# Kernel optimization log

Measured on AMD Instinct MI355X. Metric: run time of the kernel, lower is better.

## Reference

```python
import jax, jax.numpy as jnp
import numpy as np

DIM = 384
HEADS = 12
WIN = (2, 7, 7)
MLP_RATIO = 4.0
EPS = 1e-5


def _rel_index(Wt, Wh, Ww):
    t, h, w = np.meshgrid(np.arange(Wt), np.arange(Wh), np.arange(Ww), indexing='ij')
    coords = np.stack([t, h, w]).reshape(3, -1).T  # (N,3)
    rel = coords[:, None] - coords[None]  # (N,N,3)
    rel[..., 0] += Wt - 1
    rel[..., 1] += Wh - 1
    rel[..., 2] += Ww - 1
    rel[..., 0] *= (2 * Wh - 1) * (2 * Ww - 1)
    rel[..., 1] *= (2 * Ww - 1)
    return rel.sum(-1)  # (N,N) int


def setup_inputs() -> dict:
    key = jax.random.key(0)
    ks = jax.random.split(key, 16)
    d = DIM
    hdim = int(d * MLP_RATIO)
    Wt, Wh, Ww = WIN
    table_size = (2 * Wt - 1) * (2 * Wh - 1) * (2 * Ww - 1)
    s = lambda fan: 1.0 / np.sqrt(fan)
    return {
        'x': jax.random.normal(ks[0], (2, 8, 56, 56, d), jnp.float32),
        'norm1_g': jnp.ones((d,), jnp.float32),
        'norm1_b': jnp.zeros((d,), jnp.float32),
        'qkv_w': jax.random.normal(ks[1], (d, 3 * d), jnp.float32) * s(d),
        'qkv_b': jnp.zeros((3 * d,), jnp.float32),
        'proj_w': jax.random.normal(ks[2], (d, d), jnp.float32) * s(d),
        'proj_b': jnp.zeros((d,), jnp.float32),
        'bias_table': jax.random.normal(ks[3], (table_size, HEADS), jnp.float32) * 0.02,
        'norm2_g': jnp.ones((d,), jnp.float32),
        'norm2_b': jnp.zeros((d,), jnp.float32),
        'fc1_w': jax.random.normal(ks[4], (d, hdim), jnp.float32) * s(d),
        'fc1_b': jnp.zeros((hdim,), jnp.float32),
        'fc2_w': jax.random.normal(ks[5], (hdim, d), jnp.float32) * s(hdim),
        'fc2_b': jnp.zeros((d,), jnp.float32),
        'rel_index': jnp.asarray(_rel_index(*WIN), jnp.int32),
    }


def _ln(x, g, b):
    mu = x.mean(-1, keepdims=True)
    var = ((x - mu) ** 2).mean(-1, keepdims=True)
    return (x - mu) * jax.lax.rsqrt(var + EPS) * g + b


def _window_partition(x, win):
    B, T, H, W, C = x.shape
    Wt, Wh, Ww = win
    x = x.reshape(B, T // Wt, Wt, H // Wh, Wh, W // Ww, Ww, C)
    x = x.transpose(0, 1, 3, 5, 2, 4, 6, 7)
    return x.reshape(-1, Wt * Wh * Ww, C)


def _window_reverse(win_x, win, B, T, H, W):
    Wt, Wh, Ww = win
    C = win_x.shape[-1]
    x = win_x.reshape(B, T // Wt, H // Wh, W // Ww, Wt, Wh, Ww, C)
    x = x.transpose(0, 1, 4, 2, 5, 3, 6, 7)
    return x.reshape(B, T, H, W, C)


def reference(x, norm1_g, norm1_b, qkv_w, qkv_b, proj_w, proj_b, bias_table,
              norm2_g, norm2_b, fc1_w, fc1_b, fc2_w, fc2_b, rel_index):
    B, T, H, W, C = x.shape
    Wt, Wh, Ww = WIN
    N = Wt * Wh * Ww
    shift = (Wt // 2, Wh // 2, Ww // 2)
    head_dim = C // HEADS
    scale = head_dim ** -0.5

    shortcut = x
    h = _ln(x, norm1_g, norm1_b)
    h = jnp.roll(h, shift=(-shift[0], -shift[1], -shift[2]), axis=(1, 2, 3))
    # dims chosen divisible by window -> no padding branch
    wins = _window_partition(h, WIN)  # (BnW, N, C)
    BnW = wins.shape[0]

    qkv = wins @ qkv_w + qkv_b  # (BnW, N, 3C)
    qkv = qkv.reshape(BnW, N, 3, HEADS, head_dim).transpose(2, 0, 3, 1, 4)
    q, k, v = qkv[0] * scale, qkv[1], qkv[2]  # (BnW, H, N, d)

    bias = bias_table[rel_index.reshape(-1)].reshape(N, N, HEADS).transpose(2, 0, 1)
    attn = jnp.einsum('bhnd,bhmd->bhnm', q, k) + bias[None]
    attn = jax.nn.softmax(attn, axis=-1)
    out = jnp.einsum('bhnm,bhmd->bhnd', attn, v)
    out = out.transpose(0, 2, 1, 3).reshape(BnW, N, C)
    out = out @ proj_w + proj_b

    h = _window_reverse(out.reshape(-1, Wt, Wh, Ww, C), WIN, B, T, H, W)
    h = jnp.roll(h, shift=shift, axis=(1, 2, 3))
    x = shortcut + h

    h2 = _ln(x, norm2_g, norm2_b)
    h2 = jax.nn.gelu(h2 @ fc1_w + fc1_b, approximate=False) @ fc2_w + fc2_b
    return x + h2
```

## Files before the change

kernel.cpp:

```cpp
#include <hip/hip_runtime.h>
#include <cstdint>
#include <cstddef>


typedef __bf16 bf16x8 __attribute__((ext_vector_type(8)));
typedef __bf16 bf16x4 __attribute__((ext_vector_type(4)));
typedef float f32x4 __attribute__((ext_vector_type(4)));

#define DIM 384
#define QKV_DIM 1152
#define HID 1536
#define NHEADS 12
#define NTOK 50176
#define NWIN 512

__device__ __forceinline__ void gload16(const void* g, void* s) {
  __builtin_amdgcn_global_load_lds(
      (const __attribute__((address_space(1))) void*)g,
      (__attribute__((address_space(3))) void*)s, 16, 0, 0);
}

__global__ __launch_bounds__(256) void build_tokmap_k(int* __restrict__ map) {
  int t = blockIdx.x * 256 + threadIdx.x;
  if (t >= NTOK) return;
  int win = t / 98, n = t - win * 98;
  int b = win >> 8, tw = (win >> 6) & 3, hw = (win >> 3) & 7, ww = win & 7;
  int dt = n / 49; int rem = n - dt * 49; int dh = rem / 7, dw = rem - dh * 7;
  int t0 = (tw * 2 + dt + 1) & 7;
  int h0 = hw * 7 + dh + 3; if (h0 >= 56) h0 -= 56;
  int w0 = ww * 7 + dw + 3; if (w0 >= 56) w0 -= 56;
  map[t] = ((b * 8 + t0) * 56 + h0) * 56 + w0;
}

__global__ __launch_bounds__(256) void expand_biasp_k(const float* __restrict__ table,
                                                      const int* __restrict__ rel,
                                                      float* __restrict__ out) {
  int e = blockIdx.x * 256 + threadIdx.x;
  if (e >= NHEADS * 49 * 256) return;
  int r = e & 3, l = (e >> 2) & 63;
  int rest = e >> 8;
  int ni = rest % 7, mi = (rest / 7) % 7, h = rest / 49;
  int i = mi * 16 + (l >> 4) * 4 + r;
  int j = ni * 16 + (l & 15);
  float v;
  if (j >= 98) v = -1e30f;
  else if (i >= 98) v = 0.f;
  else v = table[rel[i * 98 + j] * NHEADS + h];
  out[e] = v;
}

__global__ __launch_bounds__(256) void transpose_w_k(const float* __restrict__ W,
                                                     __bf16* __restrict__ WT,
                                                     int K, int N, int scaleCols, float scale) {
  int e = blockIdx.x * 256 + threadIdx.x;
  if (e >= K * N) return;
  int n = e / K, k = e - n * K;
  float v = W[(size_t)k * N + n];
  if (n < scaleCols) v *= scale;
  WT[e] = (__bf16)v;
}

__global__ __launch_bounds__(256) void scale_bias_k(const float* __restrict__ b,
                                                    float* __restrict__ out,
                                                    int n, int scaleCols, float scale) {
  int e = blockIdx.x * 256 + threadIdx.x;
  if (e >= n) return;
  out[e] = b[e] * (e < scaleCols ? scale : 1.0f);
}

__global__ __launch_bounds__(384) void vtrans_k(const __bf16* __restrict__ qkv,
                                                __bf16* __restrict__ vt) {
  int win = blockIdx.x, t = threadIdx.x;
  const __bf16* base = qkv + (size_t)win * 98 * QKV_DIM + 768 + t;
  __bf16* orow = vt + ((size_t)win * 384 + t) * 128;
  #pragma unroll
  for (int c = 0; c < 16; ++c) {
    bf16x8 pk;
    #pragma unroll
    for (int e2 = 0; e2 < 8; ++e2) {
      int tok = c * 8 + e2;
      pk[e2] = (tok < 98) ? base[(size_t)tok * QKV_DIM] : (__bf16)0.f;
    }
    *(bf16x8*)(orow + c * 8) = pk;
  }
}

__global__ __launch_bounds__(256) void ln_k(const float* __restrict__ x,
                                            const float* __restrict__ g,
                                            const float* __restrict__ bta,
                                            __bf16* __restrict__ out,
                                            const int* __restrict__ map) {
  int w = threadIdx.x >> 6, l = threadIdx.x & 63;
  int tok = blockIdx.x * 4 + w;
  int src = map ? map[tok] : tok;
  const float* row = x + (size_t)src * DIM;
  float v[6]; float s = 0.f;
  #pragma unroll
  for (int j = 0; j < 6; ++j) { v[j] = row[l + 64 * j]; s += v[j]; }
  #pragma unroll
  for (int m = 1; m < 64; m <<= 1) s += __shfl_xor(s, m, 64);
  float mu = s * (1.f / DIM);
  float var = 0.f;
  #pragma unroll
  for (int j = 0; j < 6; ++j) { float d = v[j] - mu; var += d * d; }
  #pragma unroll
  for (int m = 1; m < 64; m <<= 1) var += __shfl_xor(var, m, 64);
  float rs = rsqrtf(var * (1.f / DIM) + 1e-5f);
  __bf16* orow = out + (size_t)tok * DIM;
  #pragma unroll
  for (int j = 0; j < 6; ++j) {
    int c = l + 64 * j;
    orow[c] = (__bf16)((v[j] - mu) * rs * g[c] + bta[c]);
  }
}

template <int EPI>
__global__ __launch_bounds__(256) void gemm_k(const __bf16* __restrict__ A,
                                              const __bf16* __restrict__ BT,
                                              const float* __restrict__ bias,
                                              int M, int N, int K,
                                              __bf16* __restrict__ outb,
                                              float* __restrict__ outf,
                                              const float* __restrict__ resid,
                                              const int* __restrict__ tokmap) {
  __shared__ __align__(1024) char lds[65536];
  const int tid = threadIdx.x;
  const int l = tid & 63, w = tid >> 6;
  const int lr = l & 15, lg = l >> 4;
  const int ntile = N >> 7;
  const int nwg8 = gridDim.x >> 3;
  const int bid = (blockIdx.x & 7) * nwg8 + (blockIdx.x >> 3);
  const int bm = bid / ntile, bn = bid - bm * ntile;
  const int m0 = bm << 7, n0 = bn << 7;
  const int wr = w >> 1, wc = w & 1;
  const int srow = l >> 3;
  const int sch = (l & 7) ^ srow;
  const __bf16* pa = A + (size_t)(m0 + w * 32 + srow) * K + sch * 8;
  const __bf16* pb = BT + (size_t)(n0 + w * 32 + srow) * K + sch * 8;
  const int doff = w * 4096;
  const int nk = K >> 6;

  #pragma unroll
  for (int i = 0; i < 4; ++i) {
    gload16(pa + (size_t)(i * 8) * K, lds + doff + i * 1024);
    gload16(pb + (size_t)(i * 8) * K, lds + 16384 + doff + i * 1024);
  }

  f32x4 acc[4][4] = {};
  for (int kt = 0; kt < nk; ++kt) {
    char* cur = lds + ((kt & 1) << 15);
    if (kt + 1 < nk) {
      char* nxt = lds + (((kt + 1) & 1) << 15);
      const size_t koff = (size_t)(kt + 1) << 6;
      #pragma unroll
      for (int i = 0; i < 4; ++i) {
        gload16(pa + (size_t)(i * 8) * K + koff, nxt + doff + i * 1024);
        gload16(pb + (size_t)(i * 8) * K + koff, nxt + 16384 + doff + i * 1024);
      }
      asm volatile("s_waitcnt vmcnt(8)" ::: "memory");
    } else {
      asm volatile("s_waitcnt vmcnt(0)" ::: "memory");
    }
    asm volatile("s_barrier" ::: "memory");
    #pragma unroll
    for (int kk = 0; kk < 2; ++kk) {
      bf16x8 af[4], bfv[4];
      const int ck = (kk << 2) + lg;
      #pragma unroll
      for (int m = 0; m < 4; ++m) {
        int r = (wr << 6) + (m << 4) + lr;
        af[m] = *(const bf16x8*)(cur + (r << 7) + ((ck ^ (r & 7)) << 4));
      }
      #pragma unroll
      for (int n = 0; n < 4; ++n) {
        int r = (wc << 6) + (n << 4) + lr;
        bfv[n] = *(const bf16x8*)(cur + 16384 + (r << 7) + ((ck ^ (r & 7)) << 4));
      }
      #pragma unroll
      for (int m = 0; m < 4; ++m)
        #pragma unroll
        for (int n = 0; n < 4; ++n)
          acc[m][n] = __builtin_amdgcn_mfma_f32_16x16x32_bf16(bfv[n], af[m], acc[m][n], 0, 0, 0);
    }
    asm volatile("s_barrier" ::: "memory");
  }

  #pragma unroll
  for (int m = 0; m < 4; ++m) {
    const int grow = m0 + (wr << 6) + (m << 4) + lr;
    #pragma unroll
    for (int n = 0; n < 4; ++n) {
      const int gcol = n0 + (wc << 6) + (n << 4) + (lg << 2);
      f32x4 a = acc[m][n] + *(const f32x4*)(bias + gcol);
      if (EPI == 0) {
        bf16x4 c;
        #pragma unroll
        for (int r = 0; r < 4; ++r) c[r] = (__bf16)a[r];
        *(bf16x4*)(outb + (size_t)grow * N + gcol) = c;
      } else if (EPI == 1) {
        int dst = tokmap[grow];
        f32x4 rv = *(const f32x4*)(resid + (size_t)dst * DIM + gcol);
        *(f32x4*)(outf + (size_t)dst * DIM + gcol) = rv + a;
      } else if (EPI == 2) {
        bf16x4 c;
        #pragma unroll
        for (int r = 0; r < 4; ++r) {
          float vv = a[r];
          float y = vv * (1.0f + 0.044715f * vv * vv);
          c[r] = (__bf16)(vv / (1.0f + __expf(-1.5957691216057308f * y)));
        }
        *(bf16x4*)(outb + (size_t)grow * N + gcol) = c;
      } else {
        f32x4 rv = *(const f32x4*)(resid + (size_t)grow * N + gcol);
        *(f32x4*)(outf + (size_t)grow * N + gcol) = rv + a;
      }
    }
  }
}

__global__ __launch_bounds__(64) void attn_k(const __bf16* __restrict__ qkv,
                                             const __bf16* __restrict__ vt,
                                             const float* __restrict__ pb,
                                             __bf16* __restrict__ out) {
  __shared__ __align__(1024) char P[4096];
  const int l = threadIdx.x, lr = l & 15, lg = l >> 4;
  const int bid = blockIdx.x;
  const int xc = bid & 7, kk = bid >> 3;
  const int wh = (kk / 7) * 8 + xc, mi = kk % 7;
  const int win = wh / NHEADS, h = wh - win * NHEADS;
  const size_t wbase = (size_t)win * 98 * QKV_DIM;
  const __bf16* qb = qkv + wbase + h * 32;
  const __bf16* kb = qb + 384;
  const bf16x8 z8 = {};
  const f32x4 fz = {};

  bf16x8 kf[7];
  #pragma unroll
  for (int ni = 0; ni < 7; ++ni) {
    int tok = ni * 16 + lr;
    kf[ni] = (tok < 98) ? *(const bf16x8*)(kb + (size_t)tok * QKV_DIM + lg * 8) : z8;
  }
  int qt = mi * 16 + lr;
  bf16x8 qf = (qt < 98) ? *(const bf16x8*)(qb + (size_t)qt * QKV_DIM + lg * 8) : z8;
  const f32x4* pbp = (const f32x4*)pb + (size_t)((h * 7 + mi) * 7) * 64 + l;
  f32x4 bv[7];
  #pragma unroll
  for (int ni = 0; ni < 7; ++ni) bv[ni] = pbp[ni * 64];

  f32x4 s[7];
  #pragma unroll
  for (int ni = 0; ni < 7; ++ni)
    s[ni] = __builtin_amdgcn_mfma_f32_16x16x32_bf16(qf, kf[ni], fz, 0, 0, 0);

  if (l < 32) {
    int row = l >> 1, c = 14 + (l & 1);
    *(f32x4*)(P + row * 256 + ((c ^ (row & 7)) << 4)) = fz;
  }

  #pragma unroll
  for (int r = 0; r < 4; ++r) {
    float mx = -1e30f;
    #pragma unroll
    for (int ni = 0; ni < 7; ++ni) {
      float vv = s[ni][r] + bv[ni][r];
      s[ni][r] = vv;
      mx = fmaxf(mx, vv);
    }
    #pragma unroll
    for (int m2 = 1; m2 < 16; m2 <<= 1) mx = fmaxf(mx, __shfl_xor(mx, m2, 64));
    float sum = 0.f;
    #pragma unroll
    for (int ni = 0; ni < 7; ++ni) { float p = __expf(s[ni][r] - mx); s[ni][r] = p; sum += p; }
    #pragma unroll
    for (int m2 = 1; m2 < 16; m2 <<= 1) sum += __shfl_xor(sum, m2, 64);
    float inv = 1.0f / sum;
    int il = lg * 4 + r;
    #pragma unroll
    for (int ni = 0; ni < 7; ++ni) {
      int j = ni * 16 + lr;
      *(__bf16*)(P + il * 256 + (((j >> 3) ^ (il & 7)) << 4) + ((j & 7) << 1)) =
          (__bf16)(s[ni][r] * inv);
    }
  }
  __syncthreads();

  bf16x8 pa[4];
  #pragma unroll
  for (int ks = 0; ks < 4; ++ks) {
    int ck = ks * 4 + lg;
    pa[ks] = *(const bf16x8*)(P + lr * 256 + ((ck ^ (lr & 7)) << 4));
  }
  const __bf16* vrow = vt + ((size_t)wh * 32) * 128;
  __bf16* ob = out + ((size_t)win * 98 + mi * 16) * DIM + h * 32;
  #pragma unroll
  for (int nf = 0; nf < 2; ++nf) {
    int d = nf * 16 + lr;
    f32x4 o = fz;
    #pragma unroll
    for (int ks = 0; ks < 4; ++ks) {
      bf16x8 vb = *(const bf16x8*)(vrow + (size_t)d * 128 + ks * 32 + lg * 8);
      o = __builtin_amdgcn_mfma_f32_16x16x32_bf16(pa[ks], vb, o, 0, 0, 0);
    }
    #pragma unroll
    for (int r = 0; r < 4; ++r) {
      int il = lg * 4 + r;
      if (mi * 16 + il < 98) ob[(size_t)il * DIM + nf * 16 + lr] = (__bf16)o[r];
    }
  }
}

extern "C" void kernel_launch(void* const* d_in, const int* in_sizes, int n_in,
                              void* d_out, int out_size, void* d_ws, size_t ws_size,
                              hipStream_t stream) {
  const float* x      = (const float*)d_in[0];
  const float* n1g    = (const float*)d_in[1];
  const float* n1b    = (const float*)d_in[2];
  const float* qkv_w  = (const float*)d_in[3];
  const float* qkv_b  = (const float*)d_in[4];
  const float* proj_w = (const float*)d_in[5];
  const float* proj_b = (const float*)d_in[6];
  const float* btab   = (const float*)d_in[7];
  const float* n2g    = (const float*)d_in[8];
  const float* n2b    = (const float*)d_in[9];
  const float* fc1_w  = (const float*)d_in[10];
  const float* fc1_b  = (const float*)d_in[11];
  const float* fc2_w  = (const float*)d_in[12];
  const float* fc2_b  = (const float*)d_in[13];
  const int*   relidx = (const int*)d_in[14];
  float* outp = (float*)d_out;
  (void)in_sizes; (void)n_in; (void)out_size; (void)ws_size;

  char* ws = (char*)d_ws;
  size_t off = 0;
  auto alloc = [&](size_t bytes) {
    char* p = ws + off;
    off = (off + bytes + 255) & ~(size_t)255;
    return p;
  };
  int*    tokmap = (int*)alloc((size_t)NTOK * 4);
  float*  biasex = (float*)alloc((size_t)NHEADS * 49 * 256 * 4);
  __bf16* wqkvT  = (__bf16*)alloc((size_t)QKV_DIM * DIM * 2);
  __bf16* wprojT = (__bf16*)alloc((size_t)DIM * DIM * 2);
  __bf16* wfc1T  = (__bf16*)alloc((size_t)HID * DIM * 2);
  __bf16* wfc2T  = (__bf16*)alloc((size_t)DIM * HID * 2);
  float*  qkvbS  = (float*)alloc((size_t)QKV_DIM * 4);
  __bf16* tokens = (__bf16*)alloc((size_t)NTOK * DIM * 2);
  __bf16* qkvbuf = (__bf16*)alloc((size_t)NTOK * HID * 2);
  __bf16* attnout = tokens;
  __bf16* h1 = qkvbuf;
  __bf16* vt = (__bf16*)d_out;

  const float scale = 0.17677669529663687f;

  build_tokmap_k<<<NTOK / 256, 256, 0, stream>>>(tokmap);
  expand_biasp_k<<<(NHEADS * 49 * 256) / 256, 256, 0, stream>>>(btab, relidx, biasex);
  transpose_w_k<<<(DIM * QKV_DIM) / 256, 256, 0, stream>>>(qkv_w, wqkvT, DIM, QKV_DIM, DIM, scale);
  transpose_w_k<<<(DIM * DIM) / 256, 256, 0, stream>>>(proj_w, wprojT, DIM, DIM, 0, 1.0f);
  transpose_w_k<<<(DIM * HID) / 256, 256, 0, stream>>>(fc1_w, wfc1T, DIM, HID, 0, 1.0f);
  transpose_w_k<<<(HID * DIM) / 256, 256, 0, stream>>>(fc2_w, wfc2T, HID, DIM, 0, 1.0f);
  scale_bias_k<<<(QKV_DIM + 255) / 256, 256, 0, stream>>>(qkv_b, qkvbS, QKV_DIM, DIM, scale);

  ln_k<<<NTOK / 4, 256, 0, stream>>>(x, n1g, n1b, tokens, tokmap);
  gemm_k<0><<<(NTOK / 128) * (QKV_DIM / 128), 256, 0, stream>>>(
      tokens, wqkvT, qkvbS, NTOK, QKV_DIM, DIM, qkvbuf, nullptr, nullptr, nullptr);
  vtrans_k<<<NWIN, 384, 0, stream>>>(qkvbuf, vt);
  attn_k<<<NWIN * NHEADS * 7, 64, 0, stream>>>(qkvbuf, vt, biasex, attnout);
  gemm_k<1><<<(NTOK / 128) * (DIM / 128), 256, 0, stream>>>(
      attnout, wprojT, proj_b, NTOK, DIM, DIM, nullptr, outp, x, tokmap);
  ln_k<<<NTOK / 4, 256, 0, stream>>>(outp, n2g, n2b, tokens, nullptr);
  gemm_k<2><<<(NTOK / 128) * (HID / 128), 256, 0, stream>>>(
      tokens, wfc1T, fc1_b, NTOK, HID, DIM, h1, nullptr, nullptr, nullptr);
  gemm_k<3><<<(NTOK / 128) * (DIM / 128), 256, 0, stream>>>(
      h1, wfc2T, fc2_b, NTOK, DIM, HID, nullptr, outp, outp, nullptr);
}
```

Measured before the change: 483.1 us.

## Add 256x256-tile 8-wave GEMM for QKV and FC1, padding QKV width to 1280

Adds a new GEMM kernel with 256x256 output tiles, 512 threads, a 128KB double-buffered LDS, prefetch loads interleaved between MFMA groups, and s_setprio raising MFMA priority. It is used for the QKV and FC1 projections. The QKV weight, bias and output stride are padded from 1152 to 1280 so the width divides into 256-wide tiles. The larger tiles aim to raise data reuse per byte loaded, at the cost of about 11% wasted QKV compute and writes, and lower occupancy.

```diff
diff --git a/kernel.cpp b/kernel.cpp
--- a/kernel.cpp
+++ b/kernel.cpp
@@ -8,7 +8,7 @@
 typedef float f32x4 __attribute__((ext_vector_type(4)));
 
 #define DIM 384
-#define QKV_DIM 1152
+#define QKV_LD 1280
 #define HID 1536
 #define NHEADS 12
 #define NTOK 50176
@@ -51,27 +51,32 @@
 
 __global__ __launch_bounds__(256) void transpose_w_k(const float* __restrict__ W,
                                                      __bf16* __restrict__ WT,
-                                                     int K, int N, int scaleCols, float scale) {
+                                                     int K, int Nreal, int Npad,
+                                                     int scaleCols, float scale) {
   int e = blockIdx.x * 256 + threadIdx.x;
-  if (e >= K * N) return;
+  if (e >= K * Npad) return;
   int n = e / K, k = e - n * K;
-  float v = W[(size_t)k * N + n];
-  if (n < scaleCols) v *= scale;
+  float v = 0.f;
+  if (n < Nreal) {
+    v = W[(size_t)k * Nreal + n];
+    if (n < scaleCols) v *= scale;
+  }
   WT[e] = (__bf16)v;
 }
 
 __global__ __launch_bounds__(256) void scale_bias_k(const float* __restrict__ b,
                                                     float* __restrict__ out,
-                                                    int n, int scaleCols, float scale) {
+                                                    int nreal, int ntot,
+                                                    int scaleCols, float scale) {
   int e = blockIdx.x * 256 + threadIdx.x;
-  if (e >= n) return;
-  out[e] = b[e] * (e < scaleCols ? scale : 1.0f);
+  if (e >= ntot) return;
+  out[e] = (e < nreal) ? b[e] * (e < scaleCols ? scale : 1.0f) : 0.f;
 }
 
 __global__ __launch_bounds__(384) void vtrans_k(const __bf16* __restrict__ qkv,
                                                 __bf16* __restrict__ vt) {
   int win = blockIdx.x, t = threadIdx.x;
-  const __bf16* base = qkv + (size_t)win * 98 * QKV_DIM + 768 + t;
+  const __bf16* base = qkv + (size_t)win * 98 * QKV_LD + 768 + t;
   __bf16* orow = vt + ((size_t)win * 384 + t) * 128;
   #pragma unroll
   for (int c = 0; c < 16; ++c) {
@@ -79,7 +84,7 @@
     #pragma unroll
     for (int e2 = 0; e2 < 8; ++e2) {
       int tok = c * 8 + e2;
-      pk[e2] = (tok < 98) ? base[(size_t)tok * QKV_DIM] : (__bf16)0.f;
+      pk[e2] = (tok < 98) ? base[(size_t)tok * QKV_LD] : (__bf16)0.f;
     }
     *(bf16x8*)(orow + c * 8) = pk;
   }
@@ -115,11 +120,133 @@
 }
 
 template <int EPI>
+__global__ __launch_bounds__(512, 2) void gemm256_k(const __bf16* __restrict__ A,
+                                                    const __bf16* __restrict__ BT,
+                                                    const float* __restrict__ bias,
+                                                    int M, int N, int K,
+                                                    __bf16* __restrict__ outb) {
+  __shared__ __align__(1024) char lds[131072];
+  const int tid = threadIdx.x;
+  const int l = tid & 63, w = tid >> 6;
+  const int lr = l & 15, lg = l >> 4;
+  const int wr = w >> 2, wc = w & 3;
+  const int ntile = N >> 8;
+  const int nwg = gridDim.x, qd = nwg >> 3, rm = nwg & 7;
+  const int xcd = blockIdx.x & 7;
+  const int wgid = (xcd < rm ? xcd * (qd + 1) : rm * (qd + 1) + (xcd - rm) * qd)
+                   + (blockIdx.x >> 3);
+  const int bm = wgid / ntile, bn = wgid - bm * ntile;
+  const int m0 = bm << 8, n0 = bn << 8;
+  const int ci3 = tid >> 3;
+  const int sch8 = ((tid & 7) ^ (ci3 & 7)) << 3;
+  const __bf16* pa = A + (size_t)(m0 + ci3) * K + sch8;
+  const __bf16* pb = BT + (size_t)(n0 + ci3) * K + sch8;
+  const int dbase = tid << 4;
+  const int nk = K >> 6;
+  const int sw0 = ((lg) ^ (lr & 7)) << 4;
+  const int sw1 = ((4 + lg) ^ (lr & 7)) << 4;
+
+  #pragma unroll
+  for (int s = 0; s < 4; ++s) {
+    gload16(pa + (size_t)(s * 64) * K, lds + s * 8192 + dbase);
+    gload16(pb + (size_t)(s * 64) * K, lds + 32768 + s * 8192 + dbase);
+  }
+
+  f32x4 acc[8][4] = {};
+
+#define LDA_(mm, sw) (*(const bf16x8*)(ab + (wr << 14) + ((mm) << 11) + (lr << 7) + (sw)))
+#define MFMA_PAIR(M0, M1, X0, X1)                                                       \
+  _Pragma("unroll")                                                                     \
+  for (int kk = 0; kk < 2; ++kk) {                                                      \
+    _Pragma("unroll")                                                                   \
+    for (int n = 0; n < 4; ++n) {                                                       \
+      acc[M0][n] = __builtin_amdgcn_mfma_f32_16x16x32_bf16(bfr[n][kk], X0[kk], acc[M0][n], 0, 0, 0); \
+      acc[M1][n] = __builtin_amdgcn_mfma_f32_16x16x32_bf16(bfr[n][kk], X1[kk], acc[M1][n], 0, 0, 0); \
+    }                                                                                   \
+  }
+
+  for (int t = 0; t < nk; ++t) {
+    const char* ab = lds + ((t & 1) << 16);
+    const char* bb = ab + 32768;
+    char* nb = lds + (((t + 1) & 1) << 16);
+    const size_t koff = (size_t)(t + 1) << 6;
+    const bool pf = (t + 1 < nk);
+    asm volatile("s_waitcnt vmcnt(0)" ::: "memory");
+    asm volatile("s_barrier" ::: "memory");
+    bf16x8 bfr[4][2];
+    #pragma unroll
+    for (int n = 0; n < 4; ++n) {
+      bfr[n][0] = *(const bf16x8*)(bb + (wc << 13) + (n << 11) + (lr << 7) + sw0);
+      bfr[n][1] = *(const bf16x8*)(bb + (wc << 13) + (n << 11) + (lr << 7) + sw1);
+    }
+    bf16x8 x0[2], x1[2];
+    x0[0] = LDA_(0, sw0); x0[1] = LDA_(0, sw1);
+    x1[0] = LDA_(1, sw0); x1[1] = LDA_(1, sw1);
+    if (pf) {
+      #pragma unroll
+      for (int s = 0; s < 4; ++s)
+        gload16(pa + (size_t)(s * 64) * K + koff, nb + s * 8192 + dbase);
+    }
+    asm volatile("s_barrier" ::: "memory");
+    __builtin_amdgcn_s_setprio(1);
+    MFMA_PAIR(0, 1, x0, x1)
+    __builtin_amdgcn_s_setprio(0);
+    x0[0] = LDA_(2, sw0); x0[1] = LDA_(2, sw1);
+    x1[0] = LDA_(3, sw0); x1[1] = LDA_(3, sw1);
+    if (pf) {
+      #pragma unroll
+      for (int s = 0; s < 4; ++s)
+        gload16(pb + (size_t)(s * 64) * K + koff, nb + 32768 + s * 8192 + dbase);
+    }
+    asm volatile("s_barrier" ::: "memory");
+    __builtin_amdgcn_s_setprio(1);
+    MFMA_PAIR(2, 3, x0, x1)
+    __builtin_amdgcn_s_setprio(0);
+    x0[0] = LDA_(4, sw0); x0[1] = LDA_(4, sw1);
+    x1[0] = LDA_(5, sw0); x1[1] = LDA_(5, sw1);
+    asm volatile("s_barrier" ::: "memory");
+    __builtin_amdgcn_s_setprio(1);
+    MFMA_PAIR(4, 5, x0, x1)
+    __builtin_amdgcn_s_setprio(0);
+    x0[0] = LDA_(6, sw0); x0[1] = LDA_(6, sw1);
+    x1[0] = LDA_(7, sw0); x1[1] = LDA_(7, sw1);
+    asm volatile("s_barrier" ::: "memory");
+    __builtin_amdgcn_s_setprio(1);
+    MFMA_PAIR(6, 7, x0, x1)
+    __builtin_amdgcn_s_setprio(0);
+  }
+#undef LDA_
+#undef MFMA_PAIR
+
+  #pragma unroll
+  for (int m = 0; m < 8; ++m) {
+    const int grow = m0 + (wr << 7) + (m << 4) + lr;
+    #pragma unroll
+    for (int n = 0; n < 4; ++n) {
+      const int gcol = n0 + (wc << 6) + (n << 4) + (lg << 2);
+      f32x4 a = acc[m][n] + *(const f32x4*)(bias + gcol);
+      bf16x4 c;
+      if (EPI == 0) {
+        #pragma unroll
+        for (int r = 0; r < 4; ++r) c[r] = (__bf16)a[r];
+      } else {
+        #pragma unroll
+        for (int r = 0; r < 4; ++r) {
+          float vv = a[r];
+          float y = vv * (1.0f + 0.044715f * vv * vv);
+          c[r] = (__bf16)(vv / (1.0f + __expf(-1.5957691216057308f * y)));
+        }
+      }
+      *(bf16x4*)(outb + (size_t)grow * N + gcol) = c;
+    }
+  }
+}
+
+template <int EPI>
 __global__ __launch_bounds__(256) void gemm_k(const __bf16* __restrict__ A,
                                               const __bf16* __restrict__ BT,
                                               const float* __restrict__ bias,
                                               int M, int N, int K,
-                                              __bf16* __restrict__ outb,
                                               float* __restrict__ outf,
                                               const float* __restrict__ resid,
                                               const int* __restrict__ tokmap) {
@@ -192,24 +319,10 @@
     for (int n = 0; n < 4; ++n) {
       const int gcol = n0 + (wc << 6) + (n << 4) + (lg << 2);
       f32x4 a = acc[m][n] + *(const f32x4*)(bias + gcol);
-      if (EPI == 0) {
-        bf16x4 c;
-        #pragma unroll
-        for (int r = 0; r < 4; ++r) c[r] = (__bf16)a[r];
-        *(bf16x4*)(outb + (size_t)grow * N + gcol) = c;
-      } else if (EPI == 1) {
+      if (EPI == 1) {
         int dst = tokmap[grow];
         f32x4 rv = *(const f32x4*)(resid + (size_t)dst * DIM + gcol);
         *(f32x4*)(outf + (size_t)dst * DIM + gcol) = rv + a;
-      } else if (EPI == 2) {
-        bf16x4 c;
-        #pragma unroll
-        for (int r = 0; r < 4; ++r) {
-          float vv = a[r];
-          float y = vv * (1.0f + 0.044715f * vv * vv);
-          c[r] = (__bf16)(vv / (1.0f + __expf(-1.5957691216057308f * y)));
-        }
-        *(bf16x4*)(outb + (size_t)grow * N + gcol) = c;
       } else {
         f32x4 rv = *(const f32x4*)(resid + (size_t)grow * N + gcol);
         *(f32x4*)(outf + (size_t)grow * N + gcol) = rv + a;
@@ -228,7 +341,7 @@
   const int xc = bid & 7, kk = bid >> 3;
   const int wh = (kk / 7) * 8 + xc, mi = kk % 7;
   const int win = wh / NHEADS, h = wh - win * NHEADS;
-  const size_t wbase = (size_t)win * 98 * QKV_DIM;
+  const size_t wbase = (size_t)win * 98 * QKV_LD;
   const __bf16* qb = qkv + wbase + h * 32;
   const __bf16* kb = qb + 384;
   const bf16x8 z8 = {};
@@ -238,10 +351,10 @@
   #pragma unroll
   for (int ni = 0; ni < 7; ++ni) {
     int tok = ni * 16 + lr;
-    kf[ni] = (tok < 98) ? *(const bf16x8*)(kb + (size_t)tok * QKV_DIM + lg * 8) : z8;
+    kf[ni] = (tok < 98) ? *(const bf16x8*)(kb + (size_t)tok * QKV_LD + lg * 8) : z8;
   }
   int qt = mi * 16 + lr;
-  bf16x8 qf = (qt < 98) ? *(const bf16x8*)(qb + (size_t)qt * QKV_DIM + lg * 8) : z8;
+  bf16x8 qf = (qt < 98) ? *(const bf16x8*)(qb + (size_t)qt * QKV_LD + lg * 8) : z8;
   const f32x4* pbp = (const f32x4*)pb + (size_t)((h * 7 + mi) * 7) * 64 + l;
   f32x4 bv[7];
   #pragma unroll
@@ -339,11 +452,11 @@
   };
   int*    tokmap = (int*)alloc((size_t)NTOK * 4);
   float*  biasex = (float*)alloc((size_t)NHEADS * 49 * 256 * 4);
-  __bf16* wqkvT  = (__bf16*)alloc((size_t)QKV_DIM * DIM * 2);
+  __bf16* wqkvT  = (__bf16*)alloc((size_t)QKV_LD * DIM * 2);
   __bf16* wprojT = (__bf16*)alloc((size_t)DIM * DIM * 2);
   __bf16* wfc1T  = (__bf16*)alloc((size_t)HID * DIM * 2);
   __bf16* wfc2T  = (__bf16*)alloc((size_t)DIM * HID * 2);
-  float*  qkvbS  = (float*)alloc((size_t)QKV_DIM * 4);
+  float*  qkvbS  = (float*)alloc((size_t)QKV_LD * 4);
   __bf16* tokens = (__bf16*)alloc((size_t)NTOK * DIM * 2);
   __bf16* qkvbuf = (__bf16*)alloc((size_t)NTOK * HID * 2);
   __bf16* attnout = tokens;
@@ -354,22 +467,22 @@
 
   build_tokmap_k<<<NTOK / 256, 256, 0, stream>>>(tokmap);
   expand_biasp_k<<<(NHEADS * 49 * 256) / 256, 256, 0, stream>>>(btab, relidx, biasex);
-  transpose_w_k<<<(DIM * QKV_DIM) / 256, 256, 0, stream>>>(qkv_w, wqkvT, DIM, QKV_DIM, DIM, scale);
-  transpose_w_k<<<(DIM * DIM) / 256, 256, 0, stream>>>(proj_w, wprojT, DIM, DIM, 0, 1.0f);
-  transpose_w_k<<<(DIM * HID) / 256, 256, 0, stream>>>(fc1_w, wfc1T, DIM, HID, 0, 1.0f);
-  transpose_w_k<<<(HID * DIM) / 256, 256, 0, stream>>>(fc2_w, wfc2T, HID, DIM, 0, 1.0f);
-  scale_bias_k<<<(QKV_DIM + 255) / 256, 256, 0, stream>>>(qkv_b, qkvbS, QKV_DIM, DIM, scale);
+  transpose_w_k<<<(DIM * QKV_LD) / 256, 256, 0, stream>>>(qkv_w, wqkvT, DIM, 1152, QKV_LD, DIM, scale);
+  transpose_w_k<<<(DIM * DIM) / 256, 256, 0, stream>>>(proj_w, wprojT, DIM, DIM, DIM, 0, 1.0f);
+  transpose_w_k<<<(DIM * HID) / 256, 256, 0, stream>>>(fc1_w, wfc1T, DIM, HID, HID, 0, 1.0f);
+  transpose_w_k<<<(HID * DIM) / 256, 256, 0, stream>>>(fc2_w, wfc2T, HID, DIM, DIM, 0, 1.0f);
+  scale_bias_k<<<(QKV_LD + 255) / 256, 256, 0, stream>>>(qkv_b, qkvbS, 1152, QKV_LD, DIM, scale);
 
   ln_k<<<NTOK / 4, 256, 0, stream>>>(x, n1g, n1b, tokens, tokmap);
-  gemm_k<0><<<(NTOK / 128) * (QKV_DIM / 128), 256, 0, stream>>>(
-      tokens, wqkvT, qkvbS, NTOK, QKV_DIM, DIM, qkvbuf, nullptr, nullptr, nullptr);
+  gemm256_k<0><<<(NTOK / 256) * (QKV_LD / 256), 512, 0, stream>>>(
+      tokens, wqkvT, qkvbS, NTOK, QKV_LD, DIM, qkvbuf);
   vtrans_k<<<NWIN, 384, 0, stream>>>(qkvbuf, vt);
   attn_k<<<NWIN * NHEADS * 7, 64, 0, stream>>>(qkvbuf, vt, biasex, attnout);
   gemm_k<1><<<(NTOK / 128) * (DIM / 128), 256, 0, stream>>>(
-      attnout, wprojT, proj_b, NTOK, DIM, DIM, nullptr, outp, x, tokmap);
+      attnout, wprojT, proj_b, NTOK, DIM, DIM, outp, x, tokmap);
   ln_k<<<NTOK / 4, 256, 0, stream>>>(outp, n2g, n2b, tokens, nullptr);
-  gemm_k<2><<<(NTOK / 128) * (HID / 128), 256, 0, stream>>>(
-      tokens, wfc1T, fc1_b, NTOK, HID, DIM, h1, nullptr, nullptr, nullptr);
+  gemm256_k<2><<<(NTOK / 256) * (HID / 256), 512, 0, stream>>>(
+      tokens, wfc1T, fc1_b, NTOK, HID, DIM, h1);
   gemm_k<3><<<(NTOK / 128) * (DIM / 128), 256, 0, stream>>>(
-      h1, wfc2T, fc2_b, NTOK, DIM, HID, nullptr, outp, outp, nullptr);
-}
+      h1, wfc2T, fc2_b, NTOK, DIM, HID, outp, outp, nullptr);
+}
```

Result: slower. 506.9 us (+4.9%).
